# Optimization experiments

Hardware: AMD Instinct MI355X
Metric: run time of the kernel (lower is better)

Reference implementation:

```python
import jax, jax.numpy as jnp
import numpy as np

B, S, H = 64, 256, 768          # batch, seq, feature_size
A = 8                            # atten_num (heads)
GNUM, GSZ = 8192, 64             # group_num, labels per group
LABELS = GNUM * GSZ              # 524288
E = 256                          # args.hidden_size (label embed dim)
TOPK = 10                        # candidates_topk


def setup_inputs() -> dict:
    key = jax.random.key(0)
    ks = jax.random.split(key, 6)
    sc = lambda d: 1.0 / np.sqrt(d)
    return {
        "inputs": jax.random.normal(ks[0], (B, S, H), jnp.float32),
        "W_att": jax.random.normal(ks[1], (A, H), jnp.float32) * sc(H),
        "b_att": jnp.zeros((A,), jnp.float32),
        "W_clf": jax.random.normal(ks[2], (GNUM, H), jnp.float32) * sc(H),
        "b_clf": jnp.zeros((GNUM,), jnp.float32),
        "W_enc": jax.random.normal(ks[3], (E, H), jnp.float32) * sc(H),
        "b_enc": jnp.zeros((E,), jnp.float32),
        "embed_table": jax.random.normal(ks[4], (LABELS, E), jnp.float32) * sc(E),
        "group_y": jnp.arange(LABELS, dtype=jnp.int32).reshape(GNUM, GSZ),
    }


def reference(inputs, W_att, b_att, W_clf, b_clf, W_enc, b_enc, embed_table, group_y):
    # MulitAttention: [B,S,H] -> atten [B,A,S] -> softmax over S -> out [B,A,H]
    atten = jnp.einsum("bsh,ah->bas", inputs, W_att) + b_att[None, :, None]
    atten_sm = jax.nn.softmax(atten, axis=-1)
    out = jnp.einsum("bas,bsh->bah", atten_sm, inputs)

    # group classifier + MaxPool1d over heads -> c_out [B, GNUM]
    group_logits = jnp.einsum("bah,gh->bag", out, W_clf) + b_clf
    c_out = jnp.max(group_logits, axis=1)

    # get_candidates (inference path): sigmoid on detached logits, topk groups,
    # gather group members (fixed group size -> regular [B, TOPK*GSZ])
    probs = jax.nn.sigmoid(jax.lax.stop_gradient(c_out))
    scores, indices = jax.lax.top_k(probs, TOPK)            # [B, TOPK]
    candidates = group_y[indices].reshape(B, TOPK * GSZ)    # [B, C]
    group_candidates_scores = jnp.repeat(scores, GSZ, axis=1)  # [B, C]

    # label scoring: encoder(out) [B,A,E], embed gather [B,C,E],
    # batched dot products [B,A,C], maxpool over heads -> l_out [B,C]
    emb = jnp.einsum("bah,eh->bae", out, W_enc) + b_enc
    embed_weights = embed_table[candidates]                 # [B, C, E]
    logits = jnp.einsum("bce,bae->bac", embed_weights, emb)
    l_out = jnp.max(logits, axis=1)

    return c_out, l_out, candidates, group_candidates_scores
```

## Files before the change

### kernel.cpp

```cpp
#include <hip/hip_runtime.h>

#define B_    64
#define S_    256
#define H_    768
#define A_    8
#define GNUM_ 8192
#define GSZ_  64
#define E_    256
#define TOPK_ 10
#define C_    (TOPK_*GSZ_)
#define BROWS (GNUM_ + E_)

typedef short  bf16x8 __attribute__((ext_vector_type(8)));
typedef float  f32x4  __attribute__((ext_vector_type(4)));

__device__ __forceinline__ ushort f2bf(float x) {
    union { float f; unsigned u; } c; c.f = x;
    unsigned r = c.u + 0x7fff + ((c.u >> 16) & 1);
    return (ushort)(r >> 16);
}
__device__ __forceinline__ float bf2f(ushort h) {
    union { float f; unsigned u; } c; c.u = ((unsigned)h) << 16;
    return c.f;
}
__device__ __forceinline__ float asf(unsigned u) {
    union { unsigned u; float f; } c; c.u = u; return c.f;
}
__device__ __forceinline__ unsigned cvt_pk_bf16(float a, float b) {
    unsigned r;
    asm("v_cvt_pk_bf16_f32 %0, %1, %2" : "=v"(r) : "v"(a), "v"(b));
    return r;
}

__global__ __launch_bounds__(256) void attn1_kernel(
    const float* __restrict__ x, const float* __restrict__ Watt,
    const float* __restrict__ batt, float* __restrict__ attT)
{
    const int b  = blockIdx.x;
    const int s0 = blockIdx.y * 64;
    const int t  = threadIdx.x;
    const int sl = t & 63;
    const int g  = __builtin_amdgcn_readfirstlane(t >> 6);
    __shared__ float Xt[64][65];
    __shared__ float Pp[8][64][5];

    const float* xb = x + ((size_t)b * S_ + s0) * H_;
    float acc[A_] = {};

    for (int h0 = 0; h0 < H_; h0 += 64) {
        __syncthreads();
#pragma unroll
        for (int i = 0; i < 4; i++) {
            int fid = i * 256 + t;
            int r = fid >> 4;
            int c = (fid & 15) * 4;
            float4 v = *(const float4*)(xb + (size_t)r * H_ + h0 + c);
            Xt[r][c] = v.x; Xt[r][c+1] = v.y; Xt[r][c+2] = v.z; Xt[r][c+3] = v.w;
        }
        __syncthreads();
        const float* wp = Watt + h0 + g * 16;
#pragma unroll
        for (int h = 0; h < 16; h++) {
            float xv = Xt[sl][g * 16 + h];
#pragma unroll
            for (int a = 0; a < A_; a++) acc[a] += xv * wp[a * H_ + h];
        }
    }
#pragma unroll
    for (int a = 0; a < A_; a++) Pp[a][sl][g] = acc[a];
    __syncthreads();
#pragma unroll
    for (int i = 0; i < 2; i++) {
        int idx = i * 256 + t;
        int a = idx >> 6, s = idx & 63;
        float v = Pp[a][s][0] + Pp[a][s][1] + Pp[a][s][2] + Pp[a][s][3] + batt[a];
        attT[(size_t)b * (S_*A_) + (size_t)(s0 + s) * A_ + a] = v;
    }
}

__global__ __launch_bounds__(256) void attn2s_kernel(
    const float* __restrict__ x, const float* __restrict__ attT,
    ushort* __restrict__ Ah, ushort* __restrict__ Al)
{
    const int b = blockIdx.x, h0 = blockIdx.y * 256, t = threadIdx.x;
    __shared__ float La[S_ * A_];
    __shared__ float Wsm[A_][260];

#pragma unroll
    for (int i = 0; i < 2; i++) {
        int fid = i * 256 + t;
        *(float4*)&La[fid * 4] =
            *(const float4*)(attT + (size_t)b * (S_*A_) + (size_t)fid * 4);
    }
    __syncthreads();

    {
        const int a = t >> 5, l = t & 31;
        float mx = -1e30f;
#pragma unroll
        for (int k = 0; k < 8; k++) mx = fmaxf(mx, La[(l + 32*k) * A_ + a]);
#pragma unroll
        for (int off = 16; off >= 1; off >>= 1) mx = fmaxf(mx, __shfl_xor(mx, off));
        float ev[8]; float sm = 0.f;
#pragma unroll
        for (int k = 0; k < 8; k++) { ev[k] = expf(La[(l + 32*k) * A_ + a] - mx); sm += ev[k]; }
#pragma unroll
        for (int off = 16; off >= 1; off >>= 1) sm += __shfl_xor(sm, off);
        float inv = 1.f / sm;
#pragma unroll
        for (int k = 0; k < 8; k++) Wsm[a][l + 32*k] = ev[k] * inv;
    }
    __syncthreads();

    const float* xb = x + (size_t)b * S_ * H_ + h0 + t;
    float o[A_] = {};
    for (int s0 = 0; s0 < S_; s0 += 4) {
        float xv0 = xb[(size_t)(s0 + 0) * H_];
        float xv1 = xb[(size_t)(s0 + 1) * H_];
        float xv2 = xb[(size_t)(s0 + 2) * H_];
        float xv3 = xb[(size_t)(s0 + 3) * H_];
#pragma unroll
        for (int a = 0; a < A_; a++) {
            float4 w = *(const float4*)&Wsm[a][s0];
            o[a] += w.x * xv0 + w.y * xv1 + w.z * xv2 + w.w * xv3;
        }
    }
#pragma unroll
    for (int a = 0; a < A_; a++) {
        float v = o[a];
        ushort hi = f2bf(v);
        ushort lo = f2bf(v - bf2f(hi));
        size_t off = (size_t)(b * 8 + a) * H_ + h0 + t;
        Ah[off] = hi; Al[off] = lo;
    }
}

__global__ __launch_bounds__(256, 1) void gemm_mfma_kernel(
    const ushort* __restrict__ Ah, const ushort* __restrict__ Al,
    const float* __restrict__ Wclf, const float* __restrict__ Wenc,
    const float* __restrict__ bclf, const float* __restrict__ benc,
    float* __restrict__ c_out, float* __restrict__ emb)
{
    const int f = blockIdx.x;
    const int xcd = f & 7, s = f >> 3;
    const int p = xcd + 8 * (s >> 2);
    const int m = s & 3;
    if (p >= BROWS / 128) return;
    const int n0 = p * 128, m0 = m * 128;

    __shared__ __align__(16) ushort lds[2][4][128 * 32];
    const int t = threadIdx.x;
    const int w = t >> 6, l = t & 63;
    const int mq = (w & 1) * 64, nq = (w >> 1) * 64;

    const int srow = t >> 2, skc = t & 3;
    const int wr_idx = ((srow * 32 + skc * 8) ^ ((srow & 7) << 3));
    const ushort* baseAh = Ah + (size_t)m0 * H_;
    const ushort* baseAl = Al + (size_t)m0 * H_;
    const float*  baseB  = (n0 < GNUM_) ? (Wclf + (size_t)n0 * H_)
                                        : (Wenc + (size_t)(n0 - GNUM_) * H_);

    uint4  stA[2][2];
    float4 stB[2][2];
    auto loadk = [&](int k0) {
        size_t oA = (size_t)srow * H_ + k0 + skc * 8;
        stA[0][0] = *(const uint4*)(baseAh + oA);
        stA[0][1] = *(const uint4*)(baseAh + oA + (size_t)64 * H_);
        stA[1][0] = *(const uint4*)(baseAl + oA);
        stA[1][1] = *(const uint4*)(baseAl + oA + (size_t)64 * H_);
        const float* bp0 = baseB + (size_t)srow * H_ + k0 + skc * 8;
        const float* bp1 = bp0 + (size_t)64 * H_;
        stB[0][0] = *(const float4*)(bp0);
        stB[0][1] = *(const float4*)(bp0 + 4);
        stB[1][0] = *(const float4*)(bp1);
        stB[1][1] = *(const float4*)(bp1 + 4);
    };

    f32x4 acc[4][4] = {};
    loadk(0);
    const int kc = l >> 4, lr = l & 15;

    for (int kt = 0; kt < H_ / 32; ++kt) {
        ushort* bufp = &lds[kt & 1][0][0];
#pragma unroll
        for (int xx = 0; xx < 2; xx++) {
            *(uint4*)(bufp + xx * 4096 + wr_idx)        = stA[xx][0];
            *(uint4*)(bufp + xx * 4096 + 2048 + wr_idx) = stA[xx][1];
        }
#pragma unroll
        for (int rp = 0; rp < 2; rp++) {
            float fv[8] = { stB[rp][0].x, stB[rp][0].y, stB[rp][0].z, stB[rp][0].w,
                            stB[rp][1].x, stB[rp][1].y, stB[rp][1].z, stB[rp][1].w };
            uint4 hi, lo;
            unsigned* hip = (unsigned*)&hi;
            unsigned* lop = (unsigned*)&lo;
#pragma unroll
            for (int j = 0; j < 4; j++) {
                unsigned pk = cvt_pk_bf16(fv[2*j], fv[2*j+1]);
                hip[j] = pk;
                float r0 = fv[2*j]   - asf(pk << 16);
                float r1 = fv[2*j+1] - asf(pk & 0xffff0000u);
                lop[j] = cvt_pk_bf16(r0, r1);
            }
            *(uint4*)(bufp + 2 * 4096 + rp * 2048 + wr_idx) = hi;
            *(uint4*)(bufp + 3 * 4096 + rp * 2048 + wr_idx) = lo;
        }
        __syncthreads();
        if (kt + 1 < H_ / 32) loadk((kt + 1) * 32);

        bf16x8 fah[4], fal[4], fbh[4], fbl[4];
#pragma unroll
        for (int mt = 0; mt < 4; mt++) {
            int r = mq + mt * 16 + lr;
            int idx = ((r * 32 + kc * 8) ^ ((r & 7) << 3));
            fah[mt] = *(const bf16x8*)(bufp + idx);
            fal[mt] = *(const bf16x8*)(bufp + 4096 + idx);
        }
#pragma unroll
        for (int nt = 0; nt < 4; nt++) {
            int r = nq + nt * 16 + lr;
            int idx = ((r * 32 + kc * 8) ^ ((r & 7) << 3));
            fbh[nt] = *(const bf16x8*)(bufp + 2 * 4096 + idx);
            fbl[nt] = *(const bf16x8*)(bufp + 3 * 4096 + idx);
        }
#pragma unroll
        for (int mt = 0; mt < 4; mt++)
#pragma unroll
            for (int nt = 0; nt < 4; nt++) {
                acc[mt][nt] = __builtin_amdgcn_mfma_f32_16x16x32_bf16(fah[mt], fbh[nt], acc[mt][nt], 0, 0, 0);
                acc[mt][nt] = __builtin_amdgcn_mfma_f32_16x16x32_bf16(fal[mt], fbh[nt], acc[mt][nt], 0, 0, 0);
                acc[mt][nt] = __builtin_amdgcn_mfma_f32_16x16x32_bf16(fah[mt], fbl[nt], acc[mt][nt], 0, 0, 0);
            }
    }

    const int q = l >> 4;
    if (n0 < GNUM_) {
#pragma unroll
        for (int mt = 0; mt < 4; mt++)
#pragma unroll
            for (int nt = 0; nt < 4; nt++) {
                f32x4 a = acc[mt][nt];
                float v = fmaxf(fmaxf(a[0], a[1]), fmaxf(a[2], a[3]));
                v = fmaxf(v, __shfl_xor(v, 16));
                if ((q & 1) == 0) {
                    int mg = m0 + mq + mt * 16 + (q >> 1) * 8;
                    int n  = n0 + nq + nt * 16 + lr;
                    c_out[(size_t)(mg >> 3) * GNUM_ + n] = v + bclf[n];
                }
            }
    } else {
#pragma unroll
        for (int mt = 0; mt < 4; mt++)
#pragma unroll
            for (int nt = 0; nt < 4; nt++) {
                int n = n0 - GNUM_ + nq + nt * 16 + lr;
                float bn = benc[n];
#pragma unroll
                for (int r2 = 0; r2 < 4; r2++) {
                    int mg = m0 + mq + mt * 16 + q * 4 + r2;
                    emb[(size_t)mg * E_ + n] = acc[mt][nt][r2] + bn;
                }
            }
    }
}

__global__ __launch_bounds__(256) void topk_kernel(
    const float* __restrict__ c_out, const int* __restrict__ gy,
    float* __restrict__ cand_f, float* __restrict__ gcs, int* __restrict__ cand_i)
{
    const int b = blockIdx.x, t = threadIdx.x;
    const int lane = t & 63, wv = t >> 6;
    __shared__ float bvv[4]; __shared__ int bii[4];
    __shared__ float topv[TOPK_]; __shared__ int topi[TOPK_];

    const float* row = c_out + (size_t)b * GNUM_;
    float lv[TOPK_]; int li[TOPK_];
#pragma unroll
    for (int k = 0; k < TOPK_; k++) { lv[k] = -1.f; li[k] = 0x7fffffff; }

    for (int i = t; i < GNUM_; i += 256) {
        float p = 1.f / (1.f + expf(-row[i]));
        if (p > lv[TOPK_ - 1]) {
            float cv = p; int ci = i;
#pragma unroll
            for (int k = 0; k < TOPK_; k++) {
                bool sw = (cv > lv[k]);
                float tv = sw ? lv[k] : cv; int ti = sw ? li[k] : ci;
                lv[k] = sw ? cv : lv[k];    li[k] = sw ? ci : li[k];
                cv = tv; ci = ti;
            }
        }
    }

    for (int rnd = 0; rnd < TOPK_; rnd++) {
        float bv = lv[0]; int bi = li[0];
#pragma unroll
        for (int off = 32; off >= 1; off >>= 1) {
            float ov = __shfl_xor(bv, off); int oi = __shfl_xor(bi, off);
            if (ov > bv || (ov == bv && oi < bi)) { bv = ov; bi = oi; }
        }
        if (lane == 0) { bvv[wv] = bv; bii[wv] = bi; }
        __syncthreads();
        float gbv = bvv[0]; int gbi = bii[0];
#pragma unroll
        for (int w = 1; w < 4; w++) {
            float ov = bvv[w]; int oi = bii[w];
            if (ov > gbv || (ov == gbv && oi < gbi)) { gbv = ov; gbi = oi; }
        }
        if (t == 0) { topv[rnd] = gbv; topi[rnd] = gbi; }
        if (li[0] == gbi) {
#pragma unroll
            for (int k = 0; k < TOPK_ - 1; k++) { lv[k] = lv[k + 1]; li[k] = li[k + 1]; }
            lv[TOPK_ - 1] = -1.f; li[TOPK_ - 1] = 0x7fffffff;
        }
        __syncthreads();
    }

    for (int j = t; j < C_; j += 256) {
        int k = j >> 6, slot = j & 63;
        int gi = topi[k];
        int lbl = gy[gi * GSZ_ + slot];
        cand_f[(size_t)b * C_ + j] = (float)lbl;
        gcs[(size_t)b * C_ + j] = topv[k];
        cand_i[b * C_ + j] = lbl;
    }
}

__global__ __launch_bounds__(256) void score_kernel(
    const float* __restrict__ embw, const float* __restrict__ et,
    const int* __restrict__ cand, float* __restrict__ l_out)
{
    const int b = blockIdx.x, c00 = blockIdx.y * 64, t = threadIdx.x;
    __shared__ float el[A_ * E_];
#pragma unroll
    for (int i = 0; i < 2; i++) {
        int fid = i * 256 + t;
        *(float4*)&el[fid * 4] = *(const float4*)(embw + (size_t)b * (A_*E_) + fid * 4);
    }
    __syncthreads();
    const int lane = t & 63, wv = t >> 6, q = lane >> 4, sub = lane & 15;

    int c = c00 + wv * 4 + q;
    const float* er = et + (size_t)cand[b * C_ + c] * E_ + sub * 4;
    float4 v0 = *(const float4*)(er);
    float4 v1 = *(const float4*)(er + 64);
    float4 v2 = *(const float4*)(er + 128);
    float4 v3 = *(const float4*)(er + 192);

    for (int it = 0; it < 4; it++) {
        float4 n0, n1, n2, n3;
        if (it + 1 < 4) {
            int cn = c00 + (it + 1) * 16 + wv * 4 + q;
            const float* ern = et + (size_t)cand[b * C_ + cn] * E_ + sub * 4;
            n0 = *(const float4*)(ern);
            n1 = *(const float4*)(ern + 64);
            n2 = *(const float4*)(ern + 128);
            n3 = *(const float4*)(ern + 192);
        }
        float best = -1e30f;
#pragma unroll
        for (int a = 0; a < A_; a++) {
            const float* ep = el + a * E_ + sub * 4;
            float4 w0 = *(const float4*)(ep);
            float4 w1 = *(const float4*)(ep + 64);
            float4 w2 = *(const float4*)(ep + 128);
            float4 w3 = *(const float4*)(ep + 192);
            float p = v0.x*w0.x + v0.y*w0.y + v0.z*w0.z + v0.w*w0.w
                    + v1.x*w1.x + v1.y*w1.y + v1.z*w1.z + v1.w*w1.w
                    + v2.x*w2.x + v2.y*w2.y + v2.z*w2.z + v2.w*w2.w
                    + v3.x*w3.x + v3.y*w3.y + v3.z*w3.z + v3.w*w3.w;
#pragma unroll
            for (int off = 8; off >= 1; off >>= 1) p += __shfl_xor(p, off);
            best = fmaxf(best, p);
        }
        if (sub == 0) l_out[(size_t)b * C_ + c00 + it * 16 + wv * 4 + q] = best;
        v0 = n0; v1 = n1; v2 = n2; v3 = n3;
    }
}

extern "C" void kernel_launch(void* const* d_in, const int* in_sizes, int n_in,
                              void* d_out, int out_size, void* d_ws, size_t ws_size,
                              hipStream_t stream)
{
    (void)in_sizes; (void)n_in; (void)out_size; (void)ws_size;
    const float* x    = (const float*)d_in[0];
    const float* Watt = (const float*)d_in[1];
    const float* batt = (const float*)d_in[2];
    const float* Wclf = (const float*)d_in[3];
    const float* bclf = (const float*)d_in[4];
    const float* Wenc = (const float*)d_in[5];
    const float* benc = (const float*)d_in[6];
    const float* et   = (const float*)d_in[7];
    const int*   gy   = (const int*)d_in[8];

    float* out    = (float*)d_out;
    float* c_out  = out;
    float* l_out  = out + (size_t)B_ * GNUM_;
    float* cand_f = l_out + (size_t)B_ * C_;
    float* gcs    = cand_f + (size_t)B_ * C_;

    char* ws = (char*)d_ws;
    float*  attT  = (float*) (ws);
    float*  embw  = (float*) (ws + 524288);
    int*    candi = (int*)   (ws + 1048576);
    ushort* Ahw   = (ushort*)(ws + 1212416);
    ushort* Alw   = (ushort*)(ws + 1998848);

    attn1_kernel<<<dim3(B_, 4), 256, 0, stream>>>(x, Watt, batt, attT);
    attn2s_kernel<<<dim3(B_, 3), 256, 0, stream>>>(x, attT, Ahw, Alw);
    gemm_mfma_kernel<<<288, 256, 0, stream>>>(Ahw, Alw, Wclf, Wenc, bclf, benc, c_out, embw);
    topk_kernel<<<B_, 256, 0, stream>>>(c_out, gy, cand_f, gcs, candi);
    score_kernel<<<dim3(B_, 10), 256, 0, stream>>>(embw, et, candi, l_out);
}
```

Baseline: 153.9 us.

## Fuse all stages into one persistent kernel with global grid barriers

Replaces the five separate launches (attention logits, softmax-weighted sum, classifier/encoder GEMM, top-k, label scoring) with one 256-block persistent kernel. The stages are separated by atomic-counter grid barriers, with a small init kernel resetting the counters. This removes per-launch overhead and the inter-kernel gaps. Work is remapped onto the fixed 256 blocks: the weighted-sum loop is software-pipelined in 16-row strips, and the encoder GEMM appears to be split out as its own phase. The risks are that spin barriers need every block co-resident, and that some stages lose parallelism, for example the GEMM drops from 288 to 256 tiles and scoring loops over chunks.

```diff
diff --git a/kernel.cpp b/kernel.cpp
--- a/kernel.cpp
+++ b/kernel.cpp
@@ -9,7 +9,7 @@
 #define E_    256
 #define TOPK_ 10
 #define C_    (TOPK_*GSZ_)
-#define BROWS (GNUM_ + E_)
+#define NBLK_ 256
 
 typedef short  bf16x8 __attribute__((ext_vector_type(8)));
 typedef float  f32x4  __attribute__((ext_vector_type(4)));
@@ -32,209 +32,225 @@
     return r;
 }
 
-__global__ __launch_bounds__(256) void attn1_kernel(
+__global__ void bar_init_kernel(unsigned* bar) {
+    if (threadIdx.x < 8) bar[threadIdx.x] = 0u;
+}
+
+__device__ __forceinline__ void gbar(unsigned* cnt) {
+    __syncthreads();
+    if (threadIdx.x == 0) {
+        __threadfence();
+        atomicAdd(cnt, 1u);
+        while (atomicAdd(cnt, 0u) < (unsigned)NBLK_) __builtin_amdgcn_s_sleep(2);
+        __threadfence();
+    }
+    __syncthreads();
+}
+
+__global__ __launch_bounds__(256, 1) void fused_kernel(
     const float* __restrict__ x, const float* __restrict__ Watt,
-    const float* __restrict__ batt, float* __restrict__ attT)
+    const float* __restrict__ batt, const float* __restrict__ Wclf,
+    const float* __restrict__ bclf, const float* __restrict__ Wenc,
+    const float* __restrict__ benc, const float* __restrict__ et,
+    const int* __restrict__ gy,
+    float* __restrict__ c_out, float* __restrict__ l_out,
+    float* __restrict__ cand_f, float* __restrict__ gcs,
+    float* __restrict__ attT, float* __restrict__ embw,
+    int* __restrict__ candi, ushort* __restrict__ Ahw, ushort* __restrict__ Alw,
+    unsigned* __restrict__ bar)
 {
-    const int b  = blockIdx.x;
-    const int s0 = blockIdx.y * 64;
-    const int t  = threadIdx.x;
-    const int sl = t & 63;
-    const int g  = __builtin_amdgcn_readfirstlane(t >> 6);
-    __shared__ float Xt[64][65];
-    __shared__ float Pp[8][64][5];
-
-    const float* xb = x + ((size_t)b * S_ + s0) * H_;
-    float acc[A_] = {};
-
-    for (int h0 = 0; h0 < H_; h0 += 64) {
+    __shared__ __align__(16) char smem[65536];
+    const int blk = blockIdx.x, t = threadIdx.x;
+
+    {
+        float* Xt = (float*)smem;
+        float* Pp = (float*)(smem + 16640);
+        const int b = blk >> 2, s0 = (blk & 3) * 64;
+        const int sl = t & 63;
+        const int g = __builtin_amdgcn_readfirstlane(t >> 6);
+        const float* xb = x + ((size_t)b * S_ + s0) * H_;
+        float acc[A_] = {};
+        for (int h0 = 0; h0 < H_; h0 += 64) {
+            __syncthreads();
+#pragma unroll
+            for (int i = 0; i < 4; i++) {
+                int fid = i * 256 + t;
+                int r = fid >> 4, c = (fid & 15) * 4;
+                float4 v = *(const float4*)(xb + (size_t)r * H_ + h0 + c);
+                Xt[r*65+c] = v.x; Xt[r*65+c+1] = v.y; Xt[r*65+c+2] = v.z; Xt[r*65+c+3] = v.w;
+            }
+            __syncthreads();
+            const float* wp = Watt + h0 + g * 16;
+#pragma unroll
+            for (int h = 0; h < 16; h++) {
+                float xv = Xt[sl*65 + g*16 + h];
+#pragma unroll
+                for (int a = 0; a < A_; a++) acc[a] += xv * wp[a * H_ + h];
+            }
+        }
+#pragma unroll
+        for (int a = 0; a < A_; a++) Pp[(a*64 + sl)*5 + g] = acc[a];
         __syncthreads();
 #pragma unroll
-        for (int i = 0; i < 4; i++) {
+        for (int i = 0; i < 2; i++) {
+            int idx = i * 256 + t;
+            int a = idx >> 6, s2 = idx & 63;
+            const float* pp = &Pp[(a*64 + s2)*5];
+            float v = pp[0] + pp[1] + pp[2] + pp[3] + batt[a];
+            attT[(size_t)b * (S_*A_) + (size_t)(s0 + s2) * A_ + a] = v;
+        }
+    }
+    gbar(bar + 0);
+
+    {
+        float* La = (float*)smem;
+        float* Wm = (float*)(smem + 8192);
+        const int b = blk >> 2, hq = blk & 3;
+#pragma unroll
+        for (int i = 0; i < 2; i++) {
             int fid = i * 256 + t;
-            int r = fid >> 4;
-            int c = (fid & 15) * 4;
-            float4 v = *(const float4*)(xb + (size_t)r * H_ + h0 + c);
-            Xt[r][c] = v.x; Xt[r][c+1] = v.y; Xt[r][c+2] = v.z; Xt[r][c+3] = v.w;
+            *(float4*)&La[fid*4] = *(const float4*)(attT + (size_t)b*(S_*A_) + (size_t)fid*4);
         }
         __syncthreads();
-        const float* wp = Watt + h0 + g * 16;
-#pragma unroll
-        for (int h = 0; h < 16; h++) {
-            float xv = Xt[sl][g * 16 + h];
-#pragma unroll
-            for (int a = 0; a < A_; a++) acc[a] += xv * wp[a * H_ + h];
-        }
-    }
-#pragma unroll
-    for (int a = 0; a < A_; a++) Pp[a][sl][g] = acc[a];
-    __syncthreads();
-#pragma unroll
-    for (int i = 0; i < 2; i++) {
-        int idx = i * 256 + t;
-        int a = idx >> 6, s = idx & 63;
-        float v = Pp[a][s][0] + Pp[a][s][1] + Pp[a][s][2] + Pp[a][s][3] + batt[a];
-        attT[(size_t)b * (S_*A_) + (size_t)(s0 + s) * A_ + a] = v;
-    }
-}
-
-__global__ __launch_bounds__(256) void attn2s_kernel(
-    const float* __restrict__ x, const float* __restrict__ attT,
-    ushort* __restrict__ Ah, ushort* __restrict__ Al)
-{
-    const int b = blockIdx.x, h0 = blockIdx.y * 256, t = threadIdx.x;
-    __shared__ float La[S_ * A_];
-    __shared__ float Wsm[A_][260];
-
-#pragma unroll
-    for (int i = 0; i < 2; i++) {
-        int fid = i * 256 + t;
-        *(float4*)&La[fid * 4] =
-            *(const float4*)(attT + (size_t)b * (S_*A_) + (size_t)fid * 4);
-    }
-    __syncthreads();
+        {
+            const int a = t >> 5, l = t & 31;
+            float mx = -1e30f;
+#pragma unroll
+            for (int k = 0; k < 8; k++) mx = fmaxf(mx, La[(l + 32*k)*A_ + a]);
+#pragma unroll
+            for (int off = 16; off >= 1; off >>= 1) mx = fmaxf(mx, __shfl_xor(mx, off));
+            float ev[8]; float sm = 0.f;
+#pragma unroll
+            for (int k = 0; k < 8; k++) { ev[k] = expf(La[(l + 32*k)*A_ + a] - mx); sm += ev[k]; }
+#pragma unroll
+            for (int off = 16; off >= 1; off >>= 1) sm += __shfl_xor(sm, off);
+            float inv = 1.f / sm;
+#pragma unroll
+            for (int k = 0; k < 8; k++) Wm[a*260 + l + 32*k] = ev[k] * inv;
+        }
+        __syncthreads();
+        if (t < 192) {
+            const float* xb = x + (size_t)b * S_ * H_ + hq * 192 + t;
+            float o[A_] = {};
+            float xb0[16], xb1[16];
+#define LOADSTRIP(buf, ks) { _Pragma("unroll") \
+            for (int i = 0; i < 16; i++) buf[i] = xb[(size_t)((ks)*16 + i) * H_]; }
+#define COMPSTRIP(buf, ks) { _Pragma("unroll") \
+            for (int sg = 0; sg < 4; sg++) { _Pragma("unroll") \
+                for (int a = 0; a < A_; a++) { \
+                    float4 w2 = *(const float4*)&Wm[a*260 + (ks)*16 + sg*4]; \
+                    o[a] += w2.x*buf[sg*4+0] + w2.y*buf[sg*4+1] \
+                          + w2.z*buf[sg*4+2] + w2.w*buf[sg*4+3]; } } }
+            LOADSTRIP(xb0, 0)
+#pragma unroll
+            for (int kp = 0; kp < 8; kp++) {
+                LOADSTRIP(xb1, 2*kp + 1)
+                COMPSTRIP(xb0, 2*kp)
+                if (kp < 7) LOADSTRIP(xb0, 2*kp + 2)
+                COMPSTRIP(xb1, 2*kp + 1)
+            }
+#undef LOADSTRIP
+#undef COMPSTRIP
+#pragma unroll
+            for (int a = 0; a < A_; a++) {
+                float v = o[a];
+                ushort hi = f2bf(v);
+                ushort lo = f2bf(v - bf2f(hi));
+                size_t off = (size_t)(b * 8 + a) * H_ + hq * 192 + t;
+                Ahw[off] = hi; Alw[off] = lo;
+            }
+        }
+    }
+    gbar(bar + 1);
 
     {
-        const int a = t >> 5, l = t & 31;
-        float mx = -1e30f;
-#pragma unroll
-        for (int k = 0; k < 8; k++) mx = fmaxf(mx, La[(l + 32*k) * A_ + a]);
-#pragma unroll
-        for (int off = 16; off >= 1; off >>= 1) mx = fmaxf(mx, __shfl_xor(mx, off));
-        float ev[8]; float sm = 0.f;
-#pragma unroll
-        for (int k = 0; k < 8; k++) { ev[k] = expf(La[(l + 32*k) * A_ + a] - mx); sm += ev[k]; }
-#pragma unroll
-        for (int off = 16; off >= 1; off >>= 1) sm += __shfl_xor(sm, off);
-        float inv = 1.f / sm;
-#pragma unroll
-        for (int k = 0; k < 8; k++) Wsm[a][l + 32*k] = ev[k] * inv;
-    }
-    __syncthreads();
-
-    const float* xb = x + (size_t)b * S_ * H_ + h0 + t;
-    float o[A_] = {};
-    for (int s0 = 0; s0 < S_; s0 += 4) {
-        float xv0 = xb[(size_t)(s0 + 0) * H_];
-        float xv1 = xb[(size_t)(s0 + 1) * H_];
-        float xv2 = xb[(size_t)(s0 + 2) * H_];
-        float xv3 = xb[(size_t)(s0 + 3) * H_];
-#pragma unroll
-        for (int a = 0; a < A_; a++) {
-            float4 w = *(const float4*)&Wsm[a][s0];
-            o[a] += w.x * xv0 + w.y * xv1 + w.z * xv2 + w.w * xv3;
-        }
-    }
-#pragma unroll
-    for (int a = 0; a < A_; a++) {
-        float v = o[a];
-        ushort hi = f2bf(v);
-        ushort lo = f2bf(v - bf2f(hi));
-        size_t off = (size_t)(b * 8 + a) * H_ + h0 + t;
-        Ah[off] = hi; Al[off] = lo;
-    }
-}
-
-__global__ __launch_bounds__(256, 1) void gemm_mfma_kernel(
-    const ushort* __restrict__ Ah, const ushort* __restrict__ Al,
-    const float* __restrict__ Wclf, const float* __restrict__ Wenc,
-    const float* __restrict__ bclf, const float* __restrict__ benc,
-    float* __restrict__ c_out, float* __restrict__ emb)
-{
-    const int f = blockIdx.x;
-    const int xcd = f & 7, s = f >> 3;
-    const int p = xcd + 8 * (s >> 2);
-    const int m = s & 3;
-    if (p >= BROWS / 128) return;
-    const int n0 = p * 128, m0 = m * 128;
-
-    __shared__ __align__(16) ushort lds[2][4][128 * 32];
-    const int t = threadIdx.x;
-    const int w = t >> 6, l = t & 63;
-    const int mq = (w & 1) * 64, nq = (w >> 1) * 64;
-
-    const int srow = t >> 2, skc = t & 3;
-    const int wr_idx = ((srow * 32 + skc * 8) ^ ((srow & 7) << 3));
-    const ushort* baseAh = Ah + (size_t)m0 * H_;
-    const ushort* baseAl = Al + (size_t)m0 * H_;
-    const float*  baseB  = (n0 < GNUM_) ? (Wclf + (size_t)n0 * H_)
-                                        : (Wenc + (size_t)(n0 - GNUM_) * H_);
-
-    uint4  stA[2][2];
-    float4 stB[2][2];
-    auto loadk = [&](int k0) {
-        size_t oA = (size_t)srow * H_ + k0 + skc * 8;
-        stA[0][0] = *(const uint4*)(baseAh + oA);
-        stA[0][1] = *(const uint4*)(baseAh + oA + (size_t)64 * H_);
-        stA[1][0] = *(const uint4*)(baseAl + oA);
-        stA[1][1] = *(const uint4*)(baseAl + oA + (size_t)64 * H_);
-        const float* bp0 = baseB + (size_t)srow * H_ + k0 + skc * 8;
-        const float* bp1 = bp0 + (size_t)64 * H_;
-        stB[0][0] = *(const float4*)(bp0);
-        stB[0][1] = *(const float4*)(bp0 + 4);
-        stB[1][0] = *(const float4*)(bp1);
-        stB[1][1] = *(const float4*)(bp1 + 4);
-    };
-
-    f32x4 acc[4][4] = {};
-    loadk(0);
-    const int kc = l >> 4, lr = l & 15;
-
-    for (int kt = 0; kt < H_ / 32; ++kt) {
-        ushort* bufp = &lds[kt & 1][0][0];
-#pragma unroll
-        for (int xx = 0; xx < 2; xx++) {
-            *(uint4*)(bufp + xx * 4096 + wr_idx)        = stA[xx][0];
-            *(uint4*)(bufp + xx * 4096 + 2048 + wr_idx) = stA[xx][1];
-        }
-#pragma unroll
-        for (int rp = 0; rp < 2; rp++) {
-            float fv[8] = { stB[rp][0].x, stB[rp][0].y, stB[rp][0].z, stB[rp][0].w,
-                            stB[rp][1].x, stB[rp][1].y, stB[rp][1].z, stB[rp][1].w };
-            uint4 hi, lo;
-            unsigned* hip = (unsigned*)&hi;
-            unsigned* lop = (unsigned*)&lo;
-#pragma unroll
-            for (int j = 0; j < 4; j++) {
-                unsigned pk = cvt_pk_bf16(fv[2*j], fv[2*j+1]);
-                hip[j] = pk;
-                float r0 = fv[2*j]   - asf(pk << 16);
-                float r1 = fv[2*j+1] - asf(pk & 0xffff0000u);
-                lop[j] = cvt_pk_bf16(r0, r1);
-            }
-            *(uint4*)(bufp + 2 * 4096 + rp * 2048 + wr_idx) = hi;
-            *(uint4*)(bufp + 3 * 4096 + rp * 2048 + wr_idx) = lo;
-        }
-        __syncthreads();
-        if (kt + 1 < H_ / 32) loadk((kt + 1) * 32);
-
-        bf16x8 fah[4], fal[4], fbh[4], fbl[4];
-#pragma unroll
-        for (int mt = 0; mt < 4; mt++) {
-            int r = mq + mt * 16 + lr;
-            int idx = ((r * 32 + kc * 8) ^ ((r & 7) << 3));
-            fah[mt] = *(const bf16x8*)(bufp + idx);
-            fal[mt] = *(const bf16x8*)(bufp + 4096 + idx);
-        }
-#pragma unroll
-        for (int nt = 0; nt < 4; nt++) {
-            int r = nq + nt * 16 + lr;
-            int idx = ((r * 32 + kc * 8) ^ ((r & 7) << 3));
-            fbh[nt] = *(const bf16x8*)(bufp + 2 * 4096 + idx);
-            fbl[nt] = *(const bf16x8*)(bufp + 3 * 4096 + idx);
-        }
-#pragma unroll
-        for (int mt = 0; mt < 4; mt++)
+        ushort* lds = (ushort*)smem;
+        const int xcd = blk & 7, sB = blk >> 3;
+        const int p = xcd + 8 * (sB >> 2);
+        const int m = sB & 3;
+        const int n0 = p * 128, m0 = m * 128;
+        const int w = t >> 6, l = t & 63;
+        const int mq = (w & 1) * 64, nq = (w >> 1) * 64;
+        const int srow = t >> 2, skc = t & 3;
+        const int wr_idx = ((srow * 32 + skc * 8) ^ ((srow & 7) << 3));
+        const ushort* baseAh = Ahw + (size_t)m0 * H_;
+        const ushort* baseAl = Alw + (size_t)m0 * H_;
+        const float*  baseB  = Wclf + (size_t)n0 * H_;
+
+        uint4  stA[2][2];
+        float4 stB[2][2];
+        auto loadk = [&](int k0) {
+            size_t oA = (size_t)srow * H_ + k0 + skc * 8;
+            stA[0][0] = *(const uint4*)(baseAh + oA);
+            stA[0][1] = *(const uint4*)(baseAh + oA + (size_t)64 * H_);
+            stA[1][0] = *(const uint4*)(baseAl + oA);
+            stA[1][1] = *(const uint4*)(baseAl + oA + (size_t)64 * H_);
+            const float* bp0 = baseB + (size_t)srow * H_ + k0 + skc * 8;
+            const float* bp1 = bp0 + (size_t)64 * H_;
+            stB[0][0] = *(const float4*)(bp0);
+            stB[0][1] = *(const float4*)(bp0 + 4);
+            stB[1][0] = *(const float4*)(bp1);
+            stB[1][1] = *(const float4*)(bp1 + 4);
+        };
+
+        f32x4 acc[4][4] = {};
+        loadk(0);
+        const int kc = l >> 4, lr = l & 15;
+
+        for (int kt = 0; kt < H_ / 32; ++kt) {
+            ushort* bufp = lds + (kt & 1) * 16384;
+#pragma unroll
+            for (int xx = 0; xx < 2; xx++) {
+                *(uint4*)(bufp + xx * 4096 + wr_idx)        = stA[xx][0];
+                *(uint4*)(bufp + xx * 4096 + 2048 + wr_idx) = stA[xx][1];
+            }
+#pragma unroll
+            for (int rp = 0; rp < 2; rp++) {
+                float fv[8] = { stB[rp][0].x, stB[rp][0].y, stB[rp][0].z, stB[rp][0].w,
+                                stB[rp][1].x, stB[rp][1].y, stB[rp][1].z, stB[rp][1].w };
+                uint4 hi, lo;
+                unsigned* hip = (unsigned*)&hi;
+                unsigned* lop = (unsigned*)&lo;
+#pragma unroll
+                for (int j = 0; j < 4; j++) {
+                    unsigned pk = cvt_pk_bf16(fv[2*j], fv[2*j+1]);
+                    hip[j] = pk;
+                    float r0 = fv[2*j]   - asf(pk << 16);
+                    float r1 = fv[2*j+1] - asf(pk & 0xffff0000u);
+                    lop[j] = cvt_pk_bf16(r0, r1);
+                }
+                *(uint4*)(bufp + 2 * 4096 + rp * 2048 + wr_idx) = hi;
+                *(uint4*)(bufp + 3 * 4096 + rp * 2048 + wr_idx) = lo;
+            }
+            __syncthreads();
+            if (kt + 1 < H_ / 32) loadk((kt + 1) * 32);
+
+            bf16x8 fah[4], fal[4], fbh[4], fbl[4];
+#pragma unroll
+            for (int mt = 0; mt < 4; mt++) {
+                int r = mq + mt * 16 + lr;
+                int idx = ((r * 32 + kc * 8) ^ ((r & 7) << 3));
+                fah[mt] = *(const bf16x8*)(bufp + idx);
+                fal[mt] = *(const bf16x8*)(bufp + 4096 + idx);
+            }
 #pragma unroll
             for (int nt = 0; nt < 4; nt++) {
-                acc[mt][nt] = __builtin_amdgcn_mfma_f32_16x16x32_bf16(fah[mt], fbh[nt], acc[mt][nt], 0, 0, 0);
-                acc[mt][nt] = __builtin_amdgcn_mfma_f32_16x16x32_bf16(fal[mt], fbh[nt], acc[mt][nt], 0, 0, 0);
-                acc[mt][nt] = __builtin_amdgcn_mfma_f32_16x16x32_bf16(fah[mt], fbl[nt], acc[mt][nt], 0, 0, 0);
-            }
-    }
-
-    const int q = l >> 4;
-    if (n0 < GNUM_) {
+                int r = nq + nt * 16 + lr;
+                int idx = ((r * 32 + kc * 8) ^ ((r & 7) << 3));
+                fbh[nt] = *(const bf16x8*)(bufp + 2 * 4096 + idx);
+                fbl[nt] = *(const bf16x8*)(bufp + 3 * 4096 + idx);
+            }
+#pragma unroll
+            for (int mt = 0; mt < 4; mt++)
+#pragma unroll
+                for (int nt = 0; nt < 4; nt++) {
+                    acc[mt][nt] = __builtin_amdgcn_mfma_f32_16x16x32_bf16(fah[mt], fbh[nt], acc[mt][nt], 0, 0, 0);
+                    acc[mt][nt] = __builtin_amdgcn_mfma_f32_16x16x32_bf16(fal[mt], fbh[nt], acc[mt][nt], 0, 0, 0);
+                    acc[mt][nt] = __builtin_amdgcn_mfma_f32_16x16x32_bf16(fah[mt], fbl[nt], acc[mt][nt], 0, 0, 0);
+                }
+        }
+
+        const int q = l >> 4;
 #pragma unroll
         for (int mt = 0; mt < 4; mt++)
 #pragma unroll
@@ -248,133 +264,199 @@
                     c_out[(size_t)(mg >> 3) * GNUM_ + n] = v + bclf[n];
                 }
             }
-    } else {
-#pragma unroll
-        for (int mt = 0; mt < 4; mt++)
-#pragma unroll
-            for (int nt = 0; nt < 4; nt++) {
-                int n = n0 - GNUM_ + nq + nt * 16 + lr;
+    }
+    gbar(bar + 2);
+
+    if (blk < 64) {
+        float* bvv  = (float*)smem;
+        int*   bii  = (int*)(smem + 16);
+        float* topv = (float*)(smem + 32);
+        int*   topi = (int*)(smem + 96);
+        const int b = blk;
+        const int lane = t & 63, wv = t >> 6;
+        const float* row = c_out + (size_t)b * GNUM_;
+        float lv[TOPK_]; int li[TOPK_];
+#pragma unroll
+        for (int k = 0; k < TOPK_; k++) { lv[k] = -1.f; li[k] = 0x7fffffff; }
+        for (int i = t; i < GNUM_; i += 256) {
+            float p = 1.f / (1.f + expf(-row[i]));
+            if (p > lv[TOPK_ - 1]) {
+                float cv = p; int ci = i;
+#pragma unroll
+                for (int k = 0; k < TOPK_; k++) {
+                    bool sw = (cv > lv[k]);
+                    float tv = sw ? lv[k] : cv; int ti = sw ? li[k] : ci;
+                    lv[k] = sw ? cv : lv[k];    li[k] = sw ? ci : li[k];
+                    cv = tv; ci = ti;
+                }
+            }
+        }
+        for (int rnd = 0; rnd < TOPK_; rnd++) {
+            float bv = lv[0]; int bi = li[0];
+#pragma unroll
+            for (int off = 32; off >= 1; off >>= 1) {
+                float ov = __shfl_xor(bv, off); int oi = __shfl_xor(bi, off);
+                if (ov > bv || (ov == bv && oi < bi)) { bv = ov; bi = oi; }
+            }
+            if (lane == 0) { bvv[wv] = bv; bii[wv] = bi; }
+            __syncthreads();
+            float gbv = bvv[0]; int gbi = bii[0];
+#pragma unroll
+            for (int w2 = 1; w2 < 4; w2++) {
+                float ov = bvv[w2]; int oi = bii[w2];
+                if (ov > gbv || (ov == gbv && oi < gbi)) { gbv = ov; gbi = oi; }
+            }
+            if (t == 0) { topv[rnd] = gbv; topi[rnd] = gbi; }
+            if (li[0] == gbi) {
+#pragma unroll
+                for (int k = 0; k < TOPK_ - 1; k++) { lv[k] = lv[k + 1]; li[k] = li[k + 1]; }
+                lv[TOPK_ - 1] = -1.f; li[TOPK_ - 1] = 0x7fffffff;
+            }
+            __syncthreads();
+        }
+        for (int j = t; j < C_; j += 256) {
+            int k = j >> 6, slot = j & 63;
+            int gi = topi[k];
+            int lbl = gy[gi * GSZ_ + slot];
+            cand_f[(size_t)b * C_ + j] = (float)lbl;
+            gcs[(size_t)b * C_ + j] = topv[k];
+            candi[b * C_ + j] = lbl;
+        }
+    } else if (blk < 96) {
+        ushort* lds = (ushort*)smem;
+        const int e = blk - 64;
+        const int m0 = (e >> 2) * 64, n0e = (e & 3) * 64;
+        const int w = t >> 6, l = t & 63;
+        const int mq = (w & 1) * 32, nq = (w >> 1) * 32;
+        const int srow = t >> 2, skc = t & 3;
+        const int wr_idx = ((srow * 32 + skc * 8) ^ ((srow & 7) << 3));
+        const ushort* baseAh = Ahw + (size_t)m0 * H_;
+        const ushort* baseAl = Alw + (size_t)m0 * H_;
+        const float*  baseB  = Wenc + (size_t)n0e * H_;
+        uint4 stA[2]; float4 stB[2];
+        auto loadk = [&](int k0) {
+            size_t oA = (size_t)srow * H_ + k0 + skc * 8;
+            stA[0] = *(const uint4*)(baseAh + oA);
+            stA[1] = *(const uint4*)(baseAl + oA);
+            const float* bp = baseB + (size_t)srow * H_ + k0 + skc * 8;
+            stB[0] = *(const float4*)(bp);
+            stB[1] = *(const float4*)(bp + 4);
+        };
+        f32x4 acc[2][2] = {};
+        loadk(0);
+        const int kc = l >> 4, lr = l & 15;
+        for (int kt = 0; kt < H_ / 32; ++kt) {
+            ushort* bufp = lds + (kt & 1) * 8192;
+            *(uint4*)(bufp + wr_idx)        = stA[0];
+            *(uint4*)(bufp + 2048 + wr_idx) = stA[1];
+            {
+                float fv[8] = { stB[0].x, stB[0].y, stB[0].z, stB[0].w,
+                                stB[1].x, stB[1].y, stB[1].z, stB[1].w };
+                uint4 hi, lo;
+                unsigned* hip = (unsigned*)&hi;
+                unsigned* lop = (unsigned*)&lo;
+#pragma unroll
+                for (int j = 0; j < 4; j++) {
+                    unsigned pk = cvt_pk_bf16(fv[2*j], fv[2*j+1]);
+                    hip[j] = pk;
+                    float r0 = fv[2*j]   - asf(pk << 16);
+                    float r1 = fv[2*j+1] - asf(pk & 0xffff0000u);
+                    lop[j] = cvt_pk_bf16(r0, r1);
+                }
+                *(uint4*)(bufp + 4096 + wr_idx) = hi;
+                *(uint4*)(bufp + 6144 + wr_idx) = lo;
+            }
+            __syncthreads();
+            if (kt + 1 < H_ / 32) loadk((kt + 1) * 32);
+            bf16x8 fah[2], fal[2], fbh[2], fbl[2];
+#pragma unroll
+            for (int mt = 0; mt < 2; mt++) {
+                int r = mq + mt * 16 + lr;
+                int idx = ((r * 32 + kc * 8) ^ ((r & 7) << 3));
+                fah[mt] = *(const bf16x8*)(bufp + idx);
+                fal[mt] = *(const bf16x8*)(bufp + 2048 + idx);
+            }
+#pragma unroll
+            for (int nt = 0; nt < 2; nt++) {
+                int r = nq + nt * 16 + lr;
+                int idx = ((r * 32 + kc * 8) ^ ((r & 7) << 3));
+                fbh[nt] = *(const bf16x8*)(bufp + 4096 + idx);
+                fbl[nt] = *(const bf16x8*)(bufp + 6144 + idx);
+            }
+#pragma unroll
+            for (int mt = 0; mt < 2; mt++)
+#pragma unroll
+                for (int nt = 0; nt < 2; nt++) {
+                    acc[mt][nt] = __builtin_amdgcn_mfma_f32_16x16x32_bf16(fah[mt], fbh[nt], acc[mt][nt], 0, 0, 0);
+                    acc[mt][nt] = __builtin_amdgcn_mfma_f32_16x16x32_bf16(fal[mt], fbh[nt], acc[mt][nt], 0, 0, 0);
+                    acc[mt][nt] = __builtin_amdgcn_mfma_f32_16x16x32_bf16(fah[mt], fbl[nt], acc[mt][nt], 0, 0, 0);
+                }
+            __syncthreads();
+        }
+        const int q = l >> 4;
+#pragma unroll
+        for (int mt = 0; mt < 2; mt++)
+#pragma unroll
+            for (int nt = 0; nt < 2; nt++) {
+                int n = n0e + nq + nt * 16 + lr;
                 float bn = benc[n];
 #pragma unroll
                 for (int r2 = 0; r2 < 4; r2++) {
                     int mg = m0 + mq + mt * 16 + q * 4 + r2;
-                    emb[(size_t)mg * E_ + n] = acc[mt][nt][r2] + bn;
-                }
-            }
-    }
-}
-
-__global__ __launch_bounds__(256) void topk_kernel(
-    const float* __restrict__ c_out, const int* __restrict__ gy,
-    float* __restrict__ cand_f, float* __restrict__ gcs, int* __restrict__ cand_i)
-{
-    const int b = blockIdx.x, t = threadIdx.x;
-    const int lane = t & 63, wv = t >> 6;
-    __shared__ float bvv[4]; __shared__ int bii[4];
-    __shared__ float topv[TOPK_]; __shared__ int topi[TOPK_];
-
-    const float* row = c_out + (size_t)b * GNUM_;
-    float lv[TOPK_]; int li[TOPK_];
-#pragma unroll
-    for (int k = 0; k < TOPK_; k++) { lv[k] = -1.f; li[k] = 0x7fffffff; }
-
-    for (int i = t; i < GNUM_; i += 256) {
-        float p = 1.f / (1.f + expf(-row[i]));
-        if (p > lv[TOPK_ - 1]) {
-            float cv = p; int ci = i;
-#pragma unroll
-            for (int k = 0; k < TOPK_; k++) {
-                bool sw = (cv > lv[k]);
-                float tv = sw ? lv[k] : cv; int ti = sw ? li[k] : ci;
-                lv[k] = sw ? cv : lv[k];    li[k] = sw ? ci : li[k];
-                cv = tv; ci = ti;
-            }
-        }
-    }
-
-    for (int rnd = 0; rnd < TOPK_; rnd++) {
-        float bv = lv[0]; int bi = li[0];
-#pragma unroll
-        for (int off = 32; off >= 1; off >>= 1) {
-            float ov = __shfl_xor(bv, off); int oi = __shfl_xor(bi, off);
-            if (ov > bv || (ov == bv && oi < bi)) { bv = ov; bi = oi; }
-        }
-        if (lane == 0) { bvv[wv] = bv; bii[wv] = bi; }
+                    embw[(size_t)mg * E_ + n] = acc[mt][nt][r2] + bn;
+                }
+            }
+    }
+    gbar(bar + 3);
+
+    {
+        float* el = (float*)smem;
+        const int b = blk & 63, cb = blk >> 6;
+#pragma unroll
+        for (int i = 0; i < 2; i++) {
+            int fid = i * 256 + t;
+            *(float4*)&el[fid * 4] = *(const float4*)(embw + (size_t)b * (A_*E_) + fid * 4);
+        }
         __syncthreads();
-        float gbv = bvv[0]; int gbi = bii[0];
-#pragma unroll
-        for (int w = 1; w < 4; w++) {
-            float ov = bvv[w]; int oi = bii[w];
-            if (ov > gbv || (ov == gbv && oi < gbi)) { gbv = ov; gbi = oi; }
-        }
-        if (t == 0) { topv[rnd] = gbv; topi[rnd] = gbi; }
-        if (li[0] == gbi) {
-#pragma unroll
-            for (int k = 0; k < TOPK_ - 1; k++) { lv[k] = lv[k + 1]; li[k] = li[k + 1]; }
-            lv[TOPK_ - 1] = -1.f; li[TOPK_ - 1] = 0x7fffffff;
-        }
-        __syncthreads();
-    }
-
-    for (int j = t; j < C_; j += 256) {
-        int k = j >> 6, slot = j & 63;
-        int gi = topi[k];
-        int lbl = gy[gi * GSZ_ + slot];
-        cand_f[(size_t)b * C_ + j] = (float)lbl;
-        gcs[(size_t)b * C_ + j] = topv[k];
-        cand_i[b * C_ + j] = lbl;
-    }
-}
-
-__global__ __launch_bounds__(256) void score_kernel(
-    const float* __restrict__ embw, const float* __restrict__ et,
-    const int* __restrict__ cand, float* __restrict__ l_out)
-{
-    const int b = blockIdx.x, c00 = blockIdx.y * 64, t = threadIdx.x;
-    __shared__ float el[A_ * E_];
-#pragma unroll
-    for (int i = 0; i < 2; i++) {
-        int fid = i * 256 + t;
-        *(float4*)&el[fid * 4] = *(const float4*)(embw + (size_t)b * (A_*E_) + fid * 4);
-    }
-    __syncthreads();
-    const int lane = t & 63, wv = t >> 6, q = lane >> 4, sub = lane & 15;
-
-    int c = c00 + wv * 4 + q;
-    const float* er = et + (size_t)cand[b * C_ + c] * E_ + sub * 4;
-    float4 v0 = *(const float4*)(er);
-    float4 v1 = *(const float4*)(er + 64);
-    float4 v2 = *(const float4*)(er + 128);
-    float4 v3 = *(const float4*)(er + 192);
-
-    for (int it = 0; it < 4; it++) {
-        float4 n0, n1, n2, n3;
-        if (it + 1 < 4) {
-            int cn = c00 + (it + 1) * 16 + wv * 4 + q;
-            const float* ern = et + (size_t)cand[b * C_ + cn] * E_ + sub * 4;
-            n0 = *(const float4*)(ern);
-            n1 = *(const float4*)(ern + 64);
-            n2 = *(const float4*)(ern + 128);
-            n3 = *(const float4*)(ern + 192);
-        }
-        float best = -1e30f;
-#pragma unroll
-        for (int a = 0; a < A_; a++) {
-            const float* ep = el + a * E_ + sub * 4;
-            float4 w0 = *(const float4*)(ep);
-            float4 w1 = *(const float4*)(ep + 64);
-            float4 w2 = *(const float4*)(ep + 128);
-            float4 w3 = *(const float4*)(ep + 192);
-            float p = v0.x*w0.x + v0.y*w0.y + v0.z*w0.z + v0.w*w0.w
-                    + v1.x*w1.x + v1.y*w1.y + v1.z*w1.z + v1.w*w1.w
-                    + v2.x*w2.x + v2.y*w2.y + v2.z*w2.z + v2.w*w2.w
-                    + v3.x*w3.x + v3.y*w3.y + v3.z*w3.z + v3.w*w3.w;
-#pragma unroll
-            for (int off = 8; off >= 1; off >>= 1) p += __shfl_xor(p, off);
-            best = fmaxf(best, p);
-        }
-        if (sub == 0) l_out[(size_t)b * C_ + c00 + it * 16 + wv * 4 + q] = best;
-        v0 = n0; v1 = n1; v2 = n2; v3 = n3;
+        const int lane = t & 63, wv = t >> 6, q = lane >> 4, sub = lane & 15;
+        for (int chunk = cb; chunk < 10; chunk += 4) {
+            const int c00 = chunk * 64;
+            int c = c00 + wv * 4 + q;
+            const float* er = et + (size_t)candi[b * C_ + c] * E_ + sub * 4;
+            float4 v0 = *(const float4*)(er);
+            float4 v1 = *(const float4*)(er + 64);
+            float4 v2 = *(const float4*)(er + 128);
+            float4 v3 = *(const float4*)(er + 192);
+            for (int it = 0; it < 4; it++) {
+                float4 p0, p1, p2, p3;
+                if (it + 1 < 4) {
+                    int cn = c00 + (it + 1) * 16 + wv * 4 + q;
+                    const float* ern = et + (size_t)candi[b * C_ + cn] * E_ + sub * 4;
+                    p0 = *(const float4*)(ern);
+                    p1 = *(const float4*)(ern + 64);
+                    p2 = *(const float4*)(ern + 128);
+                    p3 = *(const float4*)(ern + 192);
+                }
+                float best = -1e30f;
+#pragma unroll
+                for (int a = 0; a < A_; a++) {
+                    const float* ep = el + a * E_ + sub * 4;
+                    float4 w0 = *(const float4*)(ep);
+                    float4 w1 = *(const float4*)(ep + 64);
+                    float4 w2 = *(const float4*)(ep + 128);
+                    float4 w3 = *(const float4*)(ep + 192);
+                    float pp = v0.x*w0.x + v0.y*w0.y + v0.z*w0.z + v0.w*w0.w
+                             + v1.x*w1.x + v1.y*w1.y + v1.z*w1.z + v1.w*w1.w
+                             + v2.x*w2.x + v2.y*w2.y + v2.z*w2.z + v2.w*w2.w
+                             + v3.x*w3.x + v3.y*w3.y + v3.z*w3.z + v3.w*w3.w;
+#pragma unroll
+                    for (int off = 8; off >= 1; off >>= 1) pp += __shfl_xor(pp, off);
+                    best = fmaxf(best, pp);
+                }
+                if (sub == 0) l_out[(size_t)b * C_ + c00 + it * 16 + wv * 4 + q] = best;
+                v0 = p0; v1 = p1; v2 = p2; v3 = p3;
+            }
+        }
     }
 }
 
@@ -400,15 +482,15 @@
     float* gcs    = cand_f + (size_t)B_ * C_;
 
     char* ws = (char*)d_ws;
-    float*  attT  = (float*) (ws);
-    float*  embw  = (float*) (ws + 524288);
-    int*    candi = (int*)   (ws + 1048576);
-    ushort* Ahw   = (ushort*)(ws + 1212416);
-    ushort* Alw   = (ushort*)(ws + 1998848);
-
-    attn1_kernel<<<dim3(B_, 4), 256, 0, stream>>>(x, Watt, batt, attT);
-    attn2s_kernel<<<dim3(B_, 3), 256, 0, stream>>>(x, attT, Ahw, Alw);
-    gemm_mfma_kernel<<<288, 256, 0, stream>>>(Ahw, Alw, Wclf, Wenc, bclf, benc, c_out, embw);
-    topk_kernel<<<B_, 256, 0, stream>>>(c_out, gy, cand_f, gcs, candi);
-    score_kernel<<<dim3(B_, 10), 256, 0, stream>>>(embw, et, candi, l_out);
-}
+    float*    attT  = (float*)   (ws);
+    float*    embw  = (float*)   (ws + 524288);
+    int*      candi = (int*)     (ws + 1048576);
+    ushort*   Ahw   = (ushort*)  (ws + 1212416);
+    ushort*   Alw   = (ushort*)  (ws + 1998848);
+    unsigned* bar   = (unsigned*)(ws + 2785280);
+
+    bar_init_kernel<<<1, 64, 0, stream>>>(bar);
+    fused_kernel<<<NBLK_, 256, 0, stream>>>(
+        x, Watt, batt, Wclf, bclf, Wenc, benc, et, gy,
+        c_out, l_out, cand_f, gcs, attT, embw, candi, Ahw, Alw, bar);
+}
```

Result: slower. 200.4 us (+30.2%).
